# Kernel optimization log

Hardware: AMD Instinct MI355X
Metric: run time of the kernel (lower is better)

The kernel has to match this reference:

```python
import jax, jax.numpy as jnp
import numpy as np

NUM_HEADS = 8
BN_EPS = 1e-5


def setup_inputs() -> dict:
    key = jax.random.key(0)
    ks = jax.random.split(key, 8)
    B, Ct, Cs, H, W, E = 8, 256, 128, 32, 32, 256
    s = 0.05  # small init scale to keep softmax logits reasonable
    return {
        "tgt": jax.random.normal(ks[0], (B, Ct, H, W), jnp.float32),
        "src": jax.random.normal(ks[1], (B, Cs, H, W), jnp.float32),
        "kv_w": jax.random.normal(ks[2], (E, Cs), jnp.float32) * s,
        "in_proj_w": jax.random.normal(ks[3], (3 * E, E), jnp.float32) * s,
        "in_proj_b": jnp.zeros((3 * E,), jnp.float32),
        "out_proj_w": jax.random.normal(ks[4], (E, E), jnp.float32) * s,
        "out_proj_b": jnp.zeros((E,), jnp.float32),
        "fuse_w": jax.random.normal(ks[5], (Ct, E), jnp.float32) * s,
        "bn_gamma": jnp.ones((Ct,), jnp.float32),
        "bn_beta": jnp.zeros((Ct,), jnp.float32),
        "bn_mean": jnp.zeros((Ct,), jnp.float32),
        "bn_var": jnp.ones((Ct,), jnp.float32),
    }


def reference(tgt, src, kv_w, in_proj_w, in_proj_b, out_proj_w, out_proj_b,
              fuse_w, bn_gamma, bn_beta, bn_mean, bn_var):
    B, Ct, H, W = tgt.shape
    E = kv_w.shape[0]
    nH = NUM_HEADS
    hd = E // nH

    # q_proj is Identity (C_tgt == embed_dim); flatten spatial to tokens [B, Q, E]
    q_seq = tgt.reshape(B, Ct, H * W).transpose(0, 2, 1)
    # kv_proj: 1x1 conv == channel matmul; then flatten to [B, K, E]
    kv_map = jnp.einsum('bchw,ec->behw', src, kv_w)
    k_seq = kv_map.reshape(B, E, H * W).transpose(0, 2, 1)

    # nn.MultiheadAttention: packed in-projection
    Wq, Wk, Wv = in_proj_w[:E], in_proj_w[E:2 * E], in_proj_w[2 * E:]
    bq, bk, bv = in_proj_b[:E], in_proj_b[E:2 * E], in_proj_b[2 * E:]
    qp = (q_seq @ Wq.T + bq).reshape(B, -1, nH, hd).transpose(0, 2, 1, 3)  # [B,h,Q,d]
    kp = (k_seq @ Wk.T + bk).reshape(B, -1, nH, hd).transpose(0, 2, 1, 3)  # [B,h,K,d]
    vp = (k_seq @ Wv.T + bv).reshape(B, -1, nH, hd).transpose(0, 2, 1, 3)  # [B,h,K,d]

    scores = jnp.einsum('bhqd,bhkd->bhqk', qp, kp) / jnp.sqrt(jnp.float32(hd))
    attn = jax.nn.softmax(scores, axis=-1)  # [B,h,Q,K] (non-flash explicit path)

    ctx = jnp.einsum('bhqk,bhkd->bhqd', attn, vp)
    ctx = ctx.transpose(0, 2, 1, 3).reshape(B, -1, E)  # [B,Q,E]
    out_seq = ctx @ out_proj_w.T + out_proj_b

    # cached spatial key-attention map: mean over heads and queries -> [B,1,Hk,Wk]
    attn_map = attn.mean(axis=(1, 2)).reshape(B, 1, H, W)

    # back to map, fuse: 1x1 conv -> BN(eval) -> SiLU, then residual add
    out_map = out_seq.transpose(0, 2, 1).reshape(B, E, H, W)
    fused = jnp.einsum('behw,ce->bchw', out_map, fuse_w)
    inv = bn_gamma / jnp.sqrt(bn_var + BN_EPS)
    bn = (fused - bn_mean[None, :, None, None]) * inv[None, :, None, None] \
         + bn_beta[None, :, None, None]
    y = tgt + bn * jax.nn.sigmoid(bn)  # SiLU
    return y, attn_map
```

## Files before the change

### kernel.cpp

```cpp
#include <hip/hip_runtime.h>
#include <hip/hip_bf16.h>

typedef unsigned short u16;
typedef unsigned int u32;
typedef __attribute__((ext_vector_type(8))) short short8;
typedef __attribute__((ext_vector_type(4))) float f32x4;
typedef __attribute__((ext_vector_type(4))) unsigned short u16x4;
typedef __attribute__((ext_vector_type(4))) int i32x4;

static __device__ __forceinline__ u16 f2bf(float x) {
  __hip_bfloat16 b = __float2bfloat16(x);
  return *reinterpret_cast<u16*>(&b);
}
static __device__ __forceinline__ u32 fbits(float x) {
  union { float f; u32 u; } v; v.f = x; return v.u;
}
static __device__ __forceinline__ u32 pk_trunc(float lo, float hi) {
  return __builtin_amdgcn_perm(fbits(hi), fbits(lo), 0x07060302u);
}

#define QSCALE2 (0.17677669529663687f * 1.4426950408889634f)

__global__ __launch_bounds__(256) void prep_kernel(
    const float* __restrict__ in_proj_w, const float* __restrict__ in_proj_b,
    const float* __restrict__ kv_w, const float* __restrict__ fuse_w,
    const float* __restrict__ out_proj_w, const float* __restrict__ out_proj_b,
    const float* __restrict__ gamma, const float* __restrict__ beta,
    const float* __restrict__ mean, const float* __restrict__ var,
    u16* __restrict__ WqB, u16* __restrict__ WkvB, u16* __restrict__ M2B,
    float* __restrict__ qbias, float2* __restrict__ bnpk) {
  int idx = blockIdx.x * 256 + threadIdx.x;
  if (idx < 65536) {
    WqB[idx] = f2bf(in_proj_w[idx] * QSCALE2);
  } else if (idx < 131072) {
    int i = idx - 65536;
    int m = i >> 7, c = i & 127;
    const float* wrow = in_proj_w + (size_t)(256 + m) * 256;
    float s = 0.f;
    for (int e2 = 0; e2 < 256; ++e2) s += wrow[e2] * kv_w[e2 * 128 + c];
    WkvB[i] = f2bf(s);
  } else if (idx < 196608) {
    int i = idx - 131072;
    int c = i >> 8, e2 = i & 255;
    float s = 0.f;
    for (int e = 0; e < 256; ++e)
      s += fuse_w[c * 256 + e] * out_proj_w[e * 256 + e2];
    M2B[i] = f2bf(s);
  } else if (idx < 196864) {
    int c = idx - 196608;
    float fbv = 0.f;
    for (int e = 0; e < 256; ++e) fbv += fuse_w[c * 256 + e] * out_proj_b[e];
    float inv = gamma[c] * rsqrtf(var[c] + 1e-5f);
    bnpk[c] = make_float2(inv, (fbv - mean[c]) * inv + beta[c]);
    qbias[c] = in_proj_b[c] * QSCALE2;
  }
}

__global__ __launch_bounds__(256) void xpose(
    const float* __restrict__ tgt, const float* __restrict__ src,
    u16* __restrict__ tgtT, u16* __restrict__ srcT) {
  __shared__ u16 tile[64 * 65];
  int b = blockIdx.z, by = blockIdx.y, sb = blockIdx.x * 64;
  const float* X;
  u16* XT;
  int C, cb;
  if (by < 4) {
    X = tgt + (size_t)b * 256 * 1024;
    XT = tgtT + (size_t)b * 1024 * 256;
    C = 256;
    cb = by * 64;
  } else {
    X = src + (size_t)b * 128 * 1024;
    XT = srcT + (size_t)b * 1024 * 128;
    C = 128;
    cb = (by - 4) * 64;
  }
  int t = threadIdx.x;
  for (int i = t; i < 4096; i += 256) {
    int c = i >> 6, s = i & 63;
    tile[c * 65 + s] = f2bf(X[(size_t)(cb + c) * 1024 + sb + s]);
  }
  __syncthreads();
  for (int i = t; i < 4096; i += 256) {
    int s = i >> 6, c = i & 63;
    XT[(size_t)(sb + s) * C + cb + c] = tile[c * 65 + s];
  }
}

__global__ __launch_bounds__(256, 4) void qkv_gemm(
    const u16* __restrict__ tgtT, const u16* __restrict__ srcT,
    const u16* __restrict__ WqB, const u16* __restrict__ WkvB,
    const float* __restrict__ qbias, const float* __restrict__ bkv,
    u16* __restrict__ QB, u16* __restrict__ KB, u16* __restrict__ VB) {
  __shared__ __align__(16) u16 Wl[64 * 40];
  __shared__ __align__(16) u16 Xl[128 * 40];
  int b = blockIdx.z, my = blockIdx.y, n0 = blockIdx.x * 128;
  bool isQ = my < 4;
  int m0 = isQ ? my * 64 : (my - 4) * 64;
  int Kd = isQ ? 256 : 128;
  const u16* Wp = isQ ? WqB : WkvB;
  const u16* Xp = isQ ? tgtT + (size_t)b * 1024 * 256
                      : srcT + (size_t)b * 1024 * 128;
  int t = threadIdx.x, wave = t >> 6, lane = t & 63;
  int lq = lane & 15, quad = lane >> 4;
  f32x4 acc[4][2];
#pragma unroll
  for (int mt = 0; mt < 4; ++mt)
#pragma unroll
    for (int nt = 0; nt < 2; ++nt) acc[mt][nt] = (f32x4){0.f, 0.f, 0.f, 0.f};

  for (int k0 = 0; k0 < Kd; k0 += 32) {
    __syncthreads();
    {
      int row = t >> 2, seg = t & 3;
      *(short8*)&Wl[row * 40 + seg * 8] =
          *(const short8*)&Wp[(size_t)(m0 + row) * Kd + k0 + seg * 8];
    }
    for (int i = t; i < 512; i += 256) {
      int row = i >> 2, seg = i & 3;
      *(short8*)&Xl[row * 40 + seg * 8] =
          *(const short8*)&Xp[(size_t)(n0 + row) * Kd + k0 + seg * 8];
    }
    __syncthreads();
    short8 af[4], bf[2];
#pragma unroll
    for (int mt = 0; mt < 4; ++mt)
      af[mt] = *(const short8*)&Wl[(mt * 16 + lq) * 40 + quad * 8];
#pragma unroll
    for (int nt = 0; nt < 2; ++nt)
      bf[nt] = *(const short8*)&Xl[(wave * 32 + nt * 16 + lq) * 40 + quad * 8];
#pragma unroll
    for (int mt = 0; mt < 4; ++mt)
#pragma unroll
      for (int nt = 0; nt < 2; ++nt)
        acc[mt][nt] = __builtin_amdgcn_mfma_f32_16x16x32_bf16(af[mt], bf[nt],
                                                              acc[mt][nt], 0, 0, 0);
  }
  if (isQ) {
#pragma unroll
    for (int mt = 0; mt < 4; ++mt) {
      int e = m0 + mt * 16 + quad * 4;
      f32x4 bi = *(const f32x4*)&qbias[e];
#pragma unroll
      for (int nt = 0; nt < 2; ++nt) {
        int n = n0 + wave * 32 + nt * 16 + lq;
        u16x4 pk;
#pragma unroll
        for (int r = 0; r < 4; ++r) pk[r] = f2bf(acc[mt][nt][r] + bi[r]);
        *(u16x4*)&QB[((size_t)b * 1024 + n) * 256 + e] = pk;
      }
    }
  } else {
#pragma unroll
    for (int mt = 0; mt < 4; ++mt) {
      int m = m0 + mt * 16 + quad * 4;
      f32x4 bi = *(const f32x4*)&bkv[m];
#pragma unroll
      for (int nt = 0; nt < 2; ++nt) {
        int n = n0 + wave * 32 + nt * 16 + lq;
        if (m < 256) {
          int hh = m >> 5, d = m & 31;
          u16x4 pk;
#pragma unroll
          for (int r = 0; r < 4; ++r) pk[r] = f2bf(acc[mt][nt][r] + bi[r]);
          *(u16x4*)&KB[((size_t)(b * 8 + hh) * 1024 + n) * 32 + d] = pk;
        } else {
          int e = m - 256;
#pragma unroll
          for (int r = 0; r < 4; ++r)
            VB[((size_t)b * 256 + e + r) * 1024 + n] = f2bf(acc[mt][nt][r] + bi[r]);
        }
      }
    }
  }
}

__global__ __launch_bounds__(256, 4) void attn_passA(
    const u16* __restrict__ QB, const u16* __restrict__ KB,
    const u16* __restrict__ VB, u16* __restrict__ ctxB,
    float* __restrict__ linv_ws) {
  __shared__ __align__(16) u16 Klds[128 * 40];
  __shared__ __align__(16) u16 Vlds[32 * 136];
  int b = blockIdx.z, h = blockIdx.y, q0 = blockIdx.x * 64;
  int t = threadIdx.x, wave = t >> 6, lane = t & 63;
  int lq = lane & 15, quad = lane >> 4;

  const u16* Qb = QB + (size_t)b * 1024 * 256 + h * 32;
  const u16* Kb = KB + (size_t)(b * 8 + h) * 1024 * 32;
  const u16* Vb = VB + (size_t)(b * 256 + h * 32) * 1024;

  int myq = q0 + wave * 16 + lq;
  short8 qf = *(const short8*)(Qb + (size_t)myq * 256 + quad * 8);

  const f32x4 zf = (f32x4){0.f, 0.f, 0.f, 0.f};
  f32x4 O0 = zf, O1 = zf;
  float lsum = 0.f;

  for (int c0 = 0; c0 < 1024; c0 += 128) {
    __syncthreads();
    for (int i = t; i < 512; i += 256) {
      int j = i >> 2, seg = i & 3;
      int jj = j & 31, pair = j & 96;
      int m = ((jj & 4) << 2) + (((jj >> 3) & 3) << 2) + (jj & 3);
      *(short8*)&Klds[(pair + m) * 40 + seg * 8] =
          *(const short8*)(Kb + (size_t)(c0 + j) * 32 + seg * 8);
    }
    for (int i = t; i < 512; i += 256) {
      int d = i >> 4, part = i & 15;
      *(short8*)&Vlds[d * 136 + part * 8] =
          *(const short8*)(Vb + (size_t)d * 1024 + c0 + part * 8);
    }
    __syncthreads();
#pragma unroll
    for (int pair = 0; pair < 4; ++pair) {
      short8 kf0 = *(const short8*)&Klds[(pair * 32 + lq) * 40 + quad * 8];
      short8 kf1 = *(const short8*)&Klds[(pair * 32 + 16 + lq) * 40 + quad * 8];
      f32x4 s0 = __builtin_amdgcn_mfma_f32_16x16x32_bf16(kf0, qf, zf, 0, 0, 0);
      f32x4 s1 = __builtin_amdgcn_mfma_f32_16x16x32_bf16(kf1, qf, zf, 0, 0, 0);
      f32x4 e0, e1;
#pragma unroll
      for (int r = 0; r < 4; ++r) {
        e0[r] = exp2f(s0[r]);
        e1[r] = exp2f(s1[r]);
      }
      lsum += (e0[0] + e0[1]) + (e0[2] + e0[3]) +
              (e1[0] + e1[1]) + (e1[2] + e1[3]);
      i32x4 pi;
      pi[0] = (int)pk_trunc(e0[0], e0[1]);
      pi[1] = (int)pk_trunc(e0[2], e0[3]);
      pi[2] = (int)pk_trunc(e1[0], e1[1]);
      pi[3] = (int)pk_trunc(e1[2], e1[3]);
      short8 pf = *(short8*)&pi;
      short8 vf0 = *(const short8*)&Vlds[lq * 136 + pair * 32 + quad * 8];
      short8 vf1 = *(const short8*)&Vlds[(16 + lq) * 136 + pair * 32 + quad * 8];
      O0 = __builtin_amdgcn_mfma_f32_16x16x32_bf16(vf0, pf, O0, 0, 0, 0);
      O1 = __builtin_amdgcn_mfma_f32_16x16x32_bf16(vf1, pf, O1, 0, 0, 0);
    }
  }

  lsum += __shfl_xor(lsum, 16);
  lsum += __shfl_xor(lsum, 32);
  float linv = 1.f / lsum;

  u16x4 pk0, pk1;
#pragma unroll
  for (int r = 0; r < 4; ++r) {
    pk0[r] = f2bf(O0[r] * linv);
    pk1[r] = f2bf(O1[r] * linv);
  }
  u16* crow = ctxB + ((size_t)b * 1024 + myq) * 256 + h * 32 + quad * 4;
  *(u16x4*)crow = pk0;
  *(u16x4*)(crow + 16) = pk1;
  if (quad == 0) linv_ws[(size_t)(b * 8 + h) * 1024 + myq] = linv;
}

__global__ __launch_bounds__(256, 4) void colsum_kernel(
    const u16* __restrict__ QB, const u16* __restrict__ KB,
    const float* __restrict__ linv_ws, float* __restrict__ attn_out) {
  __shared__ __align__(16) u16 Klds[128 * 40];
  __shared__ float colsum[1024];
  int b = blockIdx.z, h = blockIdx.y, q0 = blockIdx.x * 128;
  int t = threadIdx.x, wave = t >> 6, lane = t & 63;
  int lq = lane & 15, quad = lane >> 4;

  const u16* Qb = QB + (size_t)b * 1024 * 256 + h * 32;
  const u16* Kb = KB + (size_t)(b * 8 + h) * 1024 * 32;
  const float* lvp = linv_ws + (size_t)(b * 8 + h) * 1024 + q0 + wave * 32;

  short8 qf2[2];
  f32x4 lv[2];
#pragma unroll
  for (int mt = 0; mt < 2; ++mt) {
    qf2[mt] = *(const short8*)(Qb + (size_t)(q0 + wave * 32 + mt * 16 + lq) * 256 + quad * 8);
    lv[mt] = *(const f32x4*)&lvp[mt * 16 + quad * 4];
  }
  for (int i = t; i < 1024; i += 256) colsum[i] = 0.f;
  const f32x4 zf = (f32x4){0.f, 0.f, 0.f, 0.f};

  for (int c0 = 0; c0 < 1024; c0 += 128) {
    __syncthreads();
    for (int i = t; i < 512; i += 256)
      *(short8*)&Klds[(i >> 2) * 40 + (i & 3) * 8] =
          *(const short8*)(Kb + (size_t)c0 * 32 + i * 8);
    __syncthreads();
#pragma unroll
    for (int nt = 0; nt < 8; ++nt) {
      short8 kf = *(const short8*)&Klds[(nt * 16 + lq) * 40 + quad * 8];
      float cs = 0.f;
#pragma unroll
      for (int mt = 0; mt < 2; ++mt) {
        f32x4 s = __builtin_amdgcn_mfma_f32_16x16x32_bf16(qf2[mt], kf, zf, 0, 0, 0);
        cs += exp2f(s[0]) * lv[mt][0] + exp2f(s[1]) * lv[mt][1] +
              exp2f(s[2]) * lv[mt][2] + exp2f(s[3]) * lv[mt][3];
      }
      cs += __shfl_xor(cs, 16);
      cs += __shfl_xor(cs, 32);
      if (quad == 0) atomicAdd(&colsum[c0 + nt * 16 + lq], cs);
    }
  }
  __syncthreads();
  for (int i = t; i < 1024; i += 256)
    atomicAdd(&attn_out[b * 1024 + i], colsum[i] * (1.f / 8192.f));
}

__global__ __launch_bounds__(256, 4) void fused_out(
    const u16* __restrict__ M2B, const u16* __restrict__ ctxB,
    const float* __restrict__ tgt, const float2* __restrict__ bnpk,
    float* __restrict__ y) {
  __shared__ __align__(16) u16 Al[64 * 40];
  __shared__ __align__(16) u16 Bl[64 * 40];
  int b = blockIdx.z, c0 = blockIdx.y * 64, s0 = blockIdx.x * 64;
  int t = threadIdx.x, wave = t >> 6, lane = t & 63;
  int lq = lane & 15, quad = lane >> 4;
  f32x4 acc[4];
#pragma unroll
  for (int mt = 0; mt < 4; ++mt) acc[mt] = (f32x4){0.f, 0.f, 0.f, 0.f};

  for (int k0 = 0; k0 < 256; k0 += 32) {
    __syncthreads();
    {
      int row = t >> 2, seg = t & 3;
      *(short8*)&Al[row * 40 + seg * 8] =
          *(const short8*)&M2B[(size_t)(c0 + row) * 256 + k0 + seg * 8];
      *(short8*)&Bl[row * 40 + seg * 8] =
          *(const short8*)&ctxB[((size_t)b * 1024 + s0 + row) * 256 + k0 + seg * 8];
    }
    __syncthreads();
    short8 bf = *(const short8*)&Bl[(wave * 16 + lq) * 40 + quad * 8];
    short8 af[4];
#pragma unroll
    for (int mt = 0; mt < 4; ++mt)
      af[mt] = *(const short8*)&Al[(mt * 16 + lq) * 40 + quad * 8];
#pragma unroll
    for (int mt = 0; mt < 4; ++mt)
      acc[mt] = __builtin_amdgcn_mfma_f32_16x16x32_bf16(af[mt], bf, acc[mt], 0, 0, 0);
  }
  int s = s0 + wave * 16 + lq;
#pragma unroll
  for (int mt = 0; mt < 4; ++mt) {
#pragma unroll
    for (int r = 0; r < 4; ++r) {
      int c = c0 + mt * 16 + quad * 4 + r;
      float2 p = bnpk[c];
      float bn = acc[mt][r] * p.x + p.y;
      float sig = 1.f / (1.f + __expf(-bn));
      size_t idx = ((size_t)b * 256 + c) * 1024 + s;
      y[idx] = tgt[idx] + bn * sig;
    }
  }
}

extern "C" void kernel_launch(void* const* d_in, const int* in_sizes, int n_in,
                              void* d_out, int out_size, void* d_ws, size_t ws_size,
                              hipStream_t stream) {
  const float* tgt = (const float*)d_in[0];
  const float* src = (const float*)d_in[1];
  const float* kv_w = (const float*)d_in[2];
  const float* in_proj_w = (const float*)d_in[3];
  const float* in_proj_b = (const float*)d_in[4];
  const float* out_proj_w = (const float*)d_in[5];
  const float* out_proj_b = (const float*)d_in[6];
  const float* fuse_w = (const float*)d_in[7];
  const float* bn_gamma = (const float*)d_in[8];
  const float* bn_beta = (const float*)d_in[9];
  const float* bn_mean = (const float*)d_in[10];
  const float* bn_var = (const float*)d_in[11];

  char* W = (char*)d_ws;
  u16* WqB = (u16*)W;
  u16* WkvB = (u16*)(W + 131072);
  u16* M2B = (u16*)(W + 262144);
  float* qbias = (float*)(W + 393216);
  float2* bnpk = (float2*)(W + 394240);
  u16* tgtT = (u16*)(W + 397312);
  u16* srcT = tgtT + 2097152;
  u16* QB = srcT + 1048576;
  u16* KB = QB + 2097152;
  u16* VB = KB + 2097152;
  u16* ctxB = VB + 2097152;
  float* linv_ws = (float*)(ctxB + 2097152);

  float* y = (float*)d_out;
  float* attn_out = y + 2097152;

  hipMemsetAsync(attn_out, 0, 8192 * sizeof(float), stream);
  prep_kernel<<<769, 256, 0, stream>>>(in_proj_w, in_proj_b, kv_w, fuse_w,
                                       out_proj_w, out_proj_b, bn_gamma, bn_beta,
                                       bn_mean, bn_var, WqB, WkvB, M2B, qbias, bnpk);
  xpose<<<dim3(16, 6, 8), 256, 0, stream>>>(tgt, src, tgtT, srcT);
  qkv_gemm<<<dim3(8, 12, 8), 256, 0, stream>>>(tgtT, srcT, WqB, WkvB, qbias,
                                               in_proj_b + 256, QB, KB, VB);
  attn_passA<<<dim3(16, 8, 8), 256, 0, stream>>>(QB, KB, VB, ctxB, linv_ws);
  colsum_kernel<<<dim3(8, 8, 8), 256, 0, stream>>>(QB, KB, linv_ws, attn_out);
  fused_out<<<dim3(16, 4, 8), 256, 0, stream>>>(M2B, ctxB, tgt, bnpk, y);
}
```

Baseline: 185.3 us.

## Use direct global-to-LDS loads in GEMM/attention kernels and merge prep with transpose

Replaces register-staged global-to-shared copies in qkv_gemm, attn_passA, colsum and fused_out with global_load_lds 16-byte direct transfers. The unpadded row layout this requires is matched by changing the K and V LDS layouts and index maps. It also merges the weight-prep kernel and the input transpose kernel into one launch to remove a kernel boundary. The risks are LDS bank conflicts from dropping the padding and correctness bugs in the remapped K key permutation and V layout.

After: 168.0 us. 1.1x faster.

```diff
diff --git a/kernel.cpp b/kernel.cpp
--- a/kernel.cpp
+++ b/kernel.cpp
@@ -18,49 +18,56 @@
 static __device__ __forceinline__ u32 pk_trunc(float lo, float hi) {
   return __builtin_amdgcn_perm(fbits(hi), fbits(lo), 0x07060302u);
 }
+static __device__ __forceinline__ void gl2lds16(const u16* g, u16* l) {
+  __builtin_amdgcn_global_load_lds(
+      (const __attribute__((address_space(1))) void*)g,
+      (__attribute__((address_space(3))) void*)l, 16, 0, 0);
+}
 
 #define QSCALE2 (0.17677669529663687f * 1.4426950408889634f)
 
-__global__ __launch_bounds__(256) void prep_kernel(
+__global__ __launch_bounds__(256) void prep_xpose(
     const float* __restrict__ in_proj_w, const float* __restrict__ in_proj_b,
     const float* __restrict__ kv_w, const float* __restrict__ fuse_w,
     const float* __restrict__ out_proj_w, const float* __restrict__ out_proj_b,
     const float* __restrict__ gamma, const float* __restrict__ beta,
     const float* __restrict__ mean, const float* __restrict__ var,
+    const float* __restrict__ tgt, const float* __restrict__ src,
     u16* __restrict__ WqB, u16* __restrict__ WkvB, u16* __restrict__ M2B,
-    float* __restrict__ qbias, float2* __restrict__ bnpk) {
-  int idx = blockIdx.x * 256 + threadIdx.x;
-  if (idx < 65536) {
-    WqB[idx] = f2bf(in_proj_w[idx] * QSCALE2);
-  } else if (idx < 131072) {
-    int i = idx - 65536;
-    int m = i >> 7, c = i & 127;
-    const float* wrow = in_proj_w + (size_t)(256 + m) * 256;
-    float s = 0.f;
-    for (int e2 = 0; e2 < 256; ++e2) s += wrow[e2] * kv_w[e2 * 128 + c];
-    WkvB[i] = f2bf(s);
-  } else if (idx < 196608) {
-    int i = idx - 131072;
-    int c = i >> 8, e2 = i & 255;
-    float s = 0.f;
-    for (int e = 0; e < 256; ++e)
-      s += fuse_w[c * 256 + e] * out_proj_w[e * 256 + e2];
-    M2B[i] = f2bf(s);
-  } else if (idx < 196864) {
-    int c = idx - 196608;
-    float fbv = 0.f;
-    for (int e = 0; e < 256; ++e) fbv += fuse_w[c * 256 + e] * out_proj_b[e];
-    float inv = gamma[c] * rsqrtf(var[c] + 1e-5f);
-    bnpk[c] = make_float2(inv, (fbv - mean[c]) * inv + beta[c]);
-    qbias[c] = in_proj_b[c] * QSCALE2;
-  }
-}
-
-__global__ __launch_bounds__(256) void xpose(
-    const float* __restrict__ tgt, const float* __restrict__ src,
+    float* __restrict__ qbias, float2* __restrict__ bnpk,
     u16* __restrict__ tgtT, u16* __restrict__ srcT) {
+  if (blockIdx.x < 769) {
+    int idx = blockIdx.x * 256 + threadIdx.x;
+    if (idx < 65536) {
+      WqB[idx] = f2bf(in_proj_w[idx] * QSCALE2);
+    } else if (idx < 131072) {
+      int i = idx - 65536;
+      int m = i >> 7, c = i & 127;
+      const float* wrow = in_proj_w + (size_t)(256 + m) * 256;
+      float s = 0.f;
+      for (int e2 = 0; e2 < 256; ++e2) s += wrow[e2] * kv_w[e2 * 128 + c];
+      WkvB[i] = f2bf(s);
+    } else if (idx < 196608) {
+      int i = idx - 131072;
+      int c = i >> 8, e2 = i & 255;
+      float s = 0.f;
+      for (int e = 0; e < 256; ++e)
+        s += fuse_w[c * 256 + e] * out_proj_w[e * 256 + e2];
+      M2B[i] = f2bf(s);
+    } else if (idx < 196864) {
+      int c = idx - 196608;
+      float fbv = 0.f;
+      for (int e = 0; e < 256; ++e) fbv += fuse_w[c * 256 + e] * out_proj_b[e];
+      float inv = gamma[c] * rsqrtf(var[c] + 1e-5f);
+      bnpk[c] = make_float2(inv, (fbv - mean[c]) * inv + beta[c]);
+      qbias[c] = in_proj_b[c] * QSCALE2;
+    }
+    return;
+  }
   __shared__ u16 tile[64 * 65];
-  int b = blockIdx.z, by = blockIdx.y, sb = blockIdx.x * 64;
+  int i0 = blockIdx.x - 769;
+  int b = i0 / 96, rem = i0 % 96;
+  int by = rem >> 4, sb = (rem & 15) * 64;
   const float* X;
   u16* XT;
   int C, cb;
@@ -92,8 +99,8 @@
     const u16* __restrict__ WqB, const u16* __restrict__ WkvB,
     const float* __restrict__ qbias, const float* __restrict__ bkv,
     u16* __restrict__ QB, u16* __restrict__ KB, u16* __restrict__ VB) {
-  __shared__ __align__(16) u16 Wl[64 * 40];
-  __shared__ __align__(16) u16 Xl[128 * 40];
+  __shared__ __align__(16) u16 Wl[64 * 32];
+  __shared__ __align__(16) u16 Xl[128 * 32];
   int b = blockIdx.z, my = blockIdx.y, n0 = blockIdx.x * 128;
   bool isQ = my < 4;
   int m0 = isQ ? my * 64 : (my - 4) * 64;
@@ -103,6 +110,7 @@
                       : srcT + (size_t)b * 1024 * 128;
   int t = threadIdx.x, wave = t >> 6, lane = t & 63;
   int lq = lane & 15, quad = lane >> 4;
+  int srow = t >> 2, sseg = t & 3;
   f32x4 acc[4][2];
 #pragma unroll
   for (int mt = 0; mt < 4; ++mt)
@@ -111,24 +119,18 @@
 
   for (int k0 = 0; k0 < Kd; k0 += 32) {
     __syncthreads();
-    {
-      int row = t >> 2, seg = t & 3;
-      *(short8*)&Wl[row * 40 + seg * 8] =
-          *(const short8*)&Wp[(size_t)(m0 + row) * Kd + k0 + seg * 8];
-    }
-    for (int i = t; i < 512; i += 256) {
-      int row = i >> 2, seg = i & 3;
-      *(short8*)&Xl[row * 40 + seg * 8] =
-          *(const short8*)&Xp[(size_t)(n0 + row) * Kd + k0 + seg * 8];
-    }
+    gl2lds16(&Wp[(size_t)(m0 + srow) * Kd + k0 + sseg * 8], &Wl[wave * 512]);
+    gl2lds16(&Xp[(size_t)(n0 + srow) * Kd + k0 + sseg * 8], &Xl[wave * 512]);
+    gl2lds16(&Xp[(size_t)(n0 + 64 + srow) * Kd + k0 + sseg * 8],
+             &Xl[2048 + wave * 512]);
     __syncthreads();
     short8 af[4], bf[2];
 #pragma unroll
     for (int mt = 0; mt < 4; ++mt)
-      af[mt] = *(const short8*)&Wl[(mt * 16 + lq) * 40 + quad * 8];
+      af[mt] = *(const short8*)&Wl[(mt * 16 + lq) * 32 + quad * 8];
 #pragma unroll
     for (int nt = 0; nt < 2; ++nt)
-      bf[nt] = *(const short8*)&Xl[(wave * 32 + nt * 16 + lq) * 40 + quad * 8];
+      bf[nt] = *(const short8*)&Xl[(wave * 32 + nt * 16 + lq) * 32 + quad * 8];
 #pragma unroll
     for (int mt = 0; mt < 4; ++mt)
 #pragma unroll
@@ -179,11 +181,12 @@
     const u16* __restrict__ QB, const u16* __restrict__ KB,
     const u16* __restrict__ VB, u16* __restrict__ ctxB,
     float* __restrict__ linv_ws) {
-  __shared__ __align__(16) u16 Klds[128 * 40];
-  __shared__ __align__(16) u16 Vlds[32 * 136];
+  __shared__ __align__(16) u16 Klds[128 * 32];
+  __shared__ __align__(16) u16 Vlds[8 * 544];
   int b = blockIdx.z, h = blockIdx.y, q0 = blockIdx.x * 64;
   int t = threadIdx.x, wave = t >> 6, lane = t & 63;
   int lq = lane & 15, quad = lane >> 4;
+  int srow = t >> 2, sseg = t & 3;
 
   const u16* Qb = QB + (size_t)b * 1024 * 256 + h * 32;
   const u16* Kb = KB + (size_t)(b * 8 + h) * 1024 * 32;
@@ -195,26 +198,23 @@
   const f32x4 zf = (f32x4){0.f, 0.f, 0.f, 0.f};
   f32x4 O0 = zf, O1 = zf;
   float lsum = 0.f;
+  int keyA = ((lq >> 2) << 3) | (lq & 3);
 
   for (int c0 = 0; c0 < 1024; c0 += 128) {
     __syncthreads();
-    for (int i = t; i < 512; i += 256) {
-      int j = i >> 2, seg = i & 3;
-      int jj = j & 31, pair = j & 96;
-      int m = ((jj & 4) << 2) + (((jj >> 3) & 3) << 2) + (jj & 3);
-      *(short8*)&Klds[(pair + m) * 40 + seg * 8] =
-          *(const short8*)(Kb + (size_t)(c0 + j) * 32 + seg * 8);
-    }
-    for (int i = t; i < 512; i += 256) {
-      int d = i >> 4, part = i & 15;
-      *(short8*)&Vlds[d * 136 + part * 8] =
-          *(const short8*)(Vb + (size_t)d * 1024 + c0 + part * 8);
+    gl2lds16(Kb + (size_t)(c0 + srow) * 32 + sseg * 8, &Klds[wave * 512]);
+    gl2lds16(Kb + (size_t)(c0 + 64 + srow) * 32 + sseg * 8, &Klds[2048 + wave * 512]);
+#pragma unroll
+    for (int c = 0; c < 2; ++c) {
+      int g = c * 4 + wave;
+      int d = g * 4 + (lane >> 4);
+      gl2lds16(Vb + (size_t)d * 1024 + c0 + (lane & 15) * 8, &Vlds[g * 544]);
     }
     __syncthreads();
 #pragma unroll
     for (int pair = 0; pair < 4; ++pair) {
-      short8 kf0 = *(const short8*)&Klds[(pair * 32 + lq) * 40 + quad * 8];
-      short8 kf1 = *(const short8*)&Klds[(pair * 32 + 16 + lq) * 40 + quad * 8];
+      short8 kf0 = *(const short8*)&Klds[(pair * 32 + keyA) * 32 + quad * 8];
+      short8 kf1 = *(const short8*)&Klds[(pair * 32 + keyA + 4) * 32 + quad * 8];
       f32x4 s0 = __builtin_amdgcn_mfma_f32_16x16x32_bf16(kf0, qf, zf, 0, 0, 0);
       f32x4 s1 = __builtin_amdgcn_mfma_f32_16x16x32_bf16(kf1, qf, zf, 0, 0, 0);
       f32x4 e0, e1;
@@ -231,8 +231,10 @@
       pi[2] = (int)pk_trunc(e1[0], e1[1]);
       pi[3] = (int)pk_trunc(e1[2], e1[3]);
       short8 pf = *(short8*)&pi;
-      short8 vf0 = *(const short8*)&Vlds[lq * 136 + pair * 32 + quad * 8];
-      short8 vf1 = *(const short8*)&Vlds[(16 + lq) * 136 + pair * 32 + quad * 8];
+      short8 vf0 = *(const short8*)&Vlds[((lq >> 2) * 544) + (lq & 3) * 128 +
+                                         pair * 32 + quad * 8];
+      short8 vf1 = *(const short8*)&Vlds[((4 + (lq >> 2)) * 544) + (lq & 3) * 128 +
+                                         pair * 32 + quad * 8];
       O0 = __builtin_amdgcn_mfma_f32_16x16x32_bf16(vf0, pf, O0, 0, 0, 0);
       O1 = __builtin_amdgcn_mfma_f32_16x16x32_bf16(vf1, pf, O1, 0, 0, 0);
     }
@@ -257,11 +259,12 @@
 __global__ __launch_bounds__(256, 4) void colsum_kernel(
     const u16* __restrict__ QB, const u16* __restrict__ KB,
     const float* __restrict__ linv_ws, float* __restrict__ attn_out) {
-  __shared__ __align__(16) u16 Klds[128 * 40];
+  __shared__ __align__(16) u16 Klds[128 * 32];
   __shared__ float colsum[1024];
   int b = blockIdx.z, h = blockIdx.y, q0 = blockIdx.x * 128;
   int t = threadIdx.x, wave = t >> 6, lane = t & 63;
   int lq = lane & 15, quad = lane >> 4;
+  int srow = t >> 2, sseg = t & 3;
 
   const u16* Qb = QB + (size_t)b * 1024 * 256 + h * 32;
   const u16* Kb = KB + (size_t)(b * 8 + h) * 1024 * 32;
@@ -279,13 +282,12 @@
 
   for (int c0 = 0; c0 < 1024; c0 += 128) {
     __syncthreads();
-    for (int i = t; i < 512; i += 256)
-      *(short8*)&Klds[(i >> 2) * 40 + (i & 3) * 8] =
-          *(const short8*)(Kb + (size_t)c0 * 32 + i * 8);
+    gl2lds16(Kb + (size_t)(c0 + srow) * 32 + sseg * 8, &Klds[wave * 512]);
+    gl2lds16(Kb + (size_t)(c0 + 64 + srow) * 32 + sseg * 8, &Klds[2048 + wave * 512]);
     __syncthreads();
 #pragma unroll
     for (int nt = 0; nt < 8; ++nt) {
-      short8 kf = *(const short8*)&Klds[(nt * 16 + lq) * 40 + quad * 8];
+      short8 kf = *(const short8*)&Klds[(nt * 16 + lq) * 32 + quad * 8];
       float cs = 0.f;
 #pragma unroll
       for (int mt = 0; mt < 2; ++mt) {
@@ -307,30 +309,27 @@
     const u16* __restrict__ M2B, const u16* __restrict__ ctxB,
     const float* __restrict__ tgt, const float2* __restrict__ bnpk,
     float* __restrict__ y) {
-  __shared__ __align__(16) u16 Al[64 * 40];
-  __shared__ __align__(16) u16 Bl[64 * 40];
+  __shared__ __align__(16) u16 Al[64 * 32];
+  __shared__ __align__(16) u16 Bl[64 * 32];
   int b = blockIdx.z, c0 = blockIdx.y * 64, s0 = blockIdx.x * 64;
   int t = threadIdx.x, wave = t >> 6, lane = t & 63;
   int lq = lane & 15, quad = lane >> 4;
+  int srow = t >> 2, sseg = t & 3;
   f32x4 acc[4];
 #pragma unroll
   for (int mt = 0; mt < 4; ++mt) acc[mt] = (f32x4){0.f, 0.f, 0.f, 0.f};
 
   for (int k0 = 0; k0 < 256; k0 += 32) {
     __syncthreads();
-    {
-      int row = t >> 2, seg = t & 3;
-      *(short8*)&Al[row * 40 + seg * 8] =
-          *(const short8*)&M2B[(size_t)(c0 + row) * 256 + k0 + seg * 8];
-      *(short8*)&Bl[row * 40 + seg * 8] =
-          *(const short8*)&ctxB[((size_t)b * 1024 + s0 + row) * 256 + k0 + seg * 8];
-    }
-    __syncthreads();
-    short8 bf = *(const short8*)&Bl[(wave * 16 + lq) * 40 + quad * 8];
+    gl2lds16(&M2B[(size_t)(c0 + srow) * 256 + k0 + sseg * 8], &Al[wave * 512]);
+    gl2lds16(&ctxB[((size_t)b * 1024 + s0 + srow) * 256 + k0 + sseg * 8],
+             &Bl[wave * 512]);
+    __syncthreads();
+    short8 bf = *(const short8*)&Bl[(wave * 16 + lq) * 32 + quad * 8];
     short8 af[4];
 #pragma unroll
     for (int mt = 0; mt < 4; ++mt)
-      af[mt] = *(const short8*)&Al[(mt * 16 + lq) * 40 + quad * 8];
+      af[mt] = *(const short8*)&Al[(mt * 16 + lq) * 32 + quad * 8];
 #pragma unroll
     for (int mt = 0; mt < 4; ++mt)
       acc[mt] = __builtin_amdgcn_mfma_f32_16x16x32_bf16(af[mt], bf, acc[mt], 0, 0, 0);
@@ -384,10 +383,10 @@
   float* attn_out = y + 2097152;
 
   hipMemsetAsync(attn_out, 0, 8192 * sizeof(float), stream);
-  prep_kernel<<<769, 256, 0, stream>>>(in_proj_w, in_proj_b, kv_w, fuse_w,
+  prep_xpose<<<1537, 256, 0, stream>>>(in_proj_w, in_proj_b, kv_w, fuse_w,
                                        out_proj_w, out_proj_b, bn_gamma, bn_beta,
-                                       bn_mean, bn_var, WqB, WkvB, M2B, qbias, bnpk);
-  xpose<<<dim3(16, 6, 8), 256, 0, stream>>>(tgt, src, tgtT, srcT);
+                                       bn_mean, bn_var, tgt, src,
+                                       WqB, WkvB, M2B, qbias, bnpk, tgtT, srcT);
   qkv_gemm<<<dim3(8, 12, 8), 256, 0, stream>>>(tgtT, srcT, WqB, WkvB, qbias,
                                                in_proj_b + 256, QB, KB, VB);
   attn_passA<<<dim3(16, 8, 8), 256, 0, stream>>>(QB, KB, VB, ctxB, linv_ws);
```
